# Optimization experiments

Hardware: AMD Instinct MI355X
Metric: run time of the kernel (lower is better)

## Reference

```python
import jax, jax.numpy as jnp
import numpy as np

WS = (7, 7, 7)          # window size (S, H, W)
NUM_HEADS = 6
DIM = 192
B_, NW = 128, 32        # total windows, windows per image (mask dim)
N = WS[0] * WS[1] * WS[2]  # 343 tokens per window


def _relative_position_index():
    # Faithful replica of the torch __init__ logic (incl. indexing='xy' and
    # the 3*W1-1 / 2*W1-1 multipliers).
    cs = np.arange(WS[0]); ch = np.arange(WS[1]); cw = np.arange(WS[2])
    coords = np.stack(np.meshgrid(cs, ch, cw, indexing='xy'))  # (3, Wh, Ws, Ww)
    cf = coords.reshape(3, -1)                                  # (3, N)
    rel = cf[:, :, None] - cf[:, None, :]                       # (3, N, N)
    rel = rel.transpose(1, 2, 0).astype(np.int64)               # (N, N, 3)
    rel[:, :, 0] += WS[0] - 1
    rel[:, :, 1] += WS[1] - 1
    rel[:, :, 2] += WS[2] - 1
    rel[:, :, 0] *= 3 * WS[1] - 1
    rel[:, :, 1] *= 2 * WS[1] - 1
    return rel.sum(-1)                                          # (N, N) int


def setup_inputs() -> dict:
    key = jax.random.key(0)
    ks = jax.random.split(key, 6)
    C = DIM
    x = jax.random.normal(ks[0], (B_, N, C), dtype=jnp.float32)
    mask = jax.random.normal(ks[1], (NW, N, N), dtype=jnp.float32)
    qkv_w = jax.random.normal(ks[2], (3 * C, C), dtype=jnp.float32) * 0.02
    qkv_b = jnp.zeros((3 * C,), dtype=jnp.float32)
    proj_w = jax.random.normal(ks[3], (C, C), dtype=jnp.float32) * 0.02
    proj_b = jnp.zeros((C,), dtype=jnp.float32)
    table_len = (2 * WS[0] - 1) * (2 * WS[1] - 1) * (2 * WS[2] - 1)
    rpb_table = jax.random.normal(ks[4], (table_len, NUM_HEADS), dtype=jnp.float32) * 0.02
    rel_index = jnp.asarray(_relative_position_index(), dtype=jnp.int32)
    return {"x": x, "mask": mask, "qkv_w": qkv_w, "qkv_b": qkv_b,
            "proj_w": proj_w, "proj_b": proj_b, "rpb_table": rpb_table,
            "rel_index": rel_index}


def reference(x, mask, qkv_w, qkv_b, proj_w, proj_b, rpb_table, rel_index):
    B, n, C = x.shape
    H = NUM_HEADS
    hd = C // H
    scale = hd ** (-0.5)
    qkv = x @ qkv_w.T + qkv_b                      # (B, N, 3C)
    qkv = qkv.reshape(B, n, 3, H, hd).transpose(2, 0, 3, 1, 4)  # (3, B, H, N, hd)
    q, k, v = qkv[0] * scale, qkv[1], qkv[2]
    attn = jnp.einsum('bhnd,bhmd->bhnm', q, k)     # (B, H, N, N)
    bias = rpb_table[rel_index.reshape(-1)].reshape(n, n, H)
    attn = attn + bias.transpose(2, 0, 1)[None]    # (B, H, N, N)
    nW = mask.shape[0]
    attn = attn.reshape(B // nW, nW, H, n, n) + mask[None, :, None]
    attn = jax.nn.softmax(attn.reshape(B, H, n, n), axis=-1)
    out = jnp.einsum('bhnm,bhmd->bhnd', attn, v)   # (B, H, N, hd)
    out = out.transpose(0, 2, 1, 3).reshape(B, n, C)
    return out @ proj_w.T + proj_b
```

## Files before the change

### kernel.cpp

```cpp
#include <hip/hip_runtime.h>
#include <hip/hip_fp16.h>
#include <hip/hip_bf16.h>
#include <stdint.h>

#define WN 343
#define NH 6
#define HD 32
#define CD 192
#define NB 128
#define NWM 32
#define BMROW 352
#define BMSLICE (11*16*BMROW)
#define BMKC (16*BMROW)
#define LOG2E 1.4426950408889634f

typedef __attribute__((ext_vector_type(8))) short short8;
typedef __attribute__((ext_vector_type(4))) float f32x4;

__device__ __forceinline__ unsigned short f2bf(float f) {
  union { float f; uint32_t u; } v; v.f = f;
  uint32_t r = v.u + 0x7fffu + ((v.u >> 16) & 1u);
  return (unsigned short)(r >> 16);
}

__device__ __forceinline__ uint32_t pk2bf(float a, float b) {
  __hip_bfloat162 h = __float22bfloat162_rn(make_float2(a, b));
  return *(uint32_t*)&h;
}

__device__ __forceinline__ uint32_t pkh2(float a, float b) {
  __half2 h; h.x = __float2half(a); h.y = __float2half(b);
  return *(uint32_t*)&h;
}

typedef const __attribute__((address_space(1))) unsigned int* gas_ptr;
typedef __attribute__((address_space(3))) unsigned int* las_ptr;
__device__ __forceinline__ void gload16(const unsigned short* g, unsigned short* l) {
  __builtin_amdgcn_global_load_lds((gas_ptr)(const void*)g, (las_ptr)(void*)l, 16, 0, 0);
}

__global__ __launch_bounds__(256) void prep_kernel(
    const float* __restrict__ wq, const float* __restrict__ wp,
    unsigned short* __restrict__ wqb, unsigned short* __restrict__ wpb,
    const int* __restrict__ rel, const float* __restrict__ rpb,
    const float* __restrict__ mask, uint32_t* __restrict__ bP,
    uint32_t* __restrict__ mP, const float* __restrict__ x,
    unsigned short* __restrict__ xb) {
  __shared__ float M[88][33];
  const int bid = blockIdx.x;
  const int tid = threadIdx.x;
  if (bid < 264) {
    const int h = bid / 44;
    const int rem = bid - h * 44;
    const int kc = rem >> 2;
    const int g = rem & 3;
    const int n0 = g * 88;
    const int k0 = kc * 32;
    for (int idx = tid; idx < 88 * 32; idx += 256) {
      int nl = idx >> 5, k = idx & 31;
      int n = n0 + nl;
      int nc = (n < WN) ? n : (WN - 1);
      M[nl][k] = (k0 + k < WN) ? rpb[rel[nc * WN + k0 + k] * NH + h] * LOG2E
                               : -30000.0f;
    }
    __syncthreads();
    uint32_t* outp = bP + (size_t)h * BMSLICE + (size_t)kc * BMKC;
    if (tid < 88) {
      const int nl = tid;
      const int n = n0 + nl;
#pragma unroll
      for (int quad = 0; quad < 4; ++quad) {
        uint4 o;
        o.x = pkh2(M[nl][quad * 8 + 0], M[nl][quad * 8 + 4]);
        o.y = pkh2(M[nl][quad * 8 + 1], M[nl][quad * 8 + 5]);
        o.z = pkh2(M[nl][quad * 8 + 2], M[nl][quad * 8 + 6]);
        o.w = pkh2(M[nl][quad * 8 + 3], M[nl][quad * 8 + 7]);
        *(uint4*)(outp + ((size_t)quad * 352 + n) * 4) = o;
      }
    }
    return;
  }
  int cb = bid - 264;
  if (cb < 352) {
    const int wdx = cb / 11;
    const int kc = cb - wdx * 11;
    const int k0 = kc * 32;
    const float* mw = mask + (size_t)wdx * (WN * WN);
    uint32_t* outp = mP + (size_t)wdx * BMSLICE + (size_t)kc * BMKC;
#pragma unroll
    for (int quad = 0; quad < 4; ++quad) {
      const int q8 = quad * 8;
#pragma unroll
      for (int j = 0; j < 2; ++j) {
        int n = tid + 256 * j;
        if (n < 352) {
          float v[8];
#pragma unroll
          for (int i = 0; i < 8; ++i) {
            int kk = k0 + q8 + i;
            v[i] = (n < WN && kk < WN) ? mw[n * WN + kk] * LOG2E : 0.0f;
          }
          uint4 o;
          o.x = pkh2(v[0], v[4]);
          o.y = pkh2(v[1], v[5]);
          o.z = pkh2(v[2], v[6]);
          o.w = pkh2(v[3], v[7]);
          *(uint4*)(outp + ((size_t)quad * 352 + n) * 4) = o;
        }
      }
    }
    return;
  }
  cb -= 352;
  if (cb < 54) {
    int g = cb * 256 + tid;
    int sk = g / 768; int rem = g - sk * 768;
    int row = rem >> 2; int cc = rem & 3;
    int s = sk / 6; int kt = sk - s * 6;
    int lch = cc ^ ((row >> 1) & 3);
    const float* src = wq + (size_t)(s * 192 + row) * CD + kt * 32 + lch * 8;
    f32x4 a = *(const f32x4*)src;
    f32x4 b = *(const f32x4*)(src + 4);
    union { short8 v8; uint32_t d[4]; } pk;
    pk.d[0] = pk2bf(a[0], a[1]);
    pk.d[1] = pk2bf(a[2], a[3]);
    pk.d[2] = pk2bf(b[0], b[1]);
    pk.d[3] = pk2bf(b[2], b[3]);
    *(short8*)(wqb + (size_t)g * 8) = pk.v8;
    return;
  }
  cb -= 54;
  if (cb < 18) {
    int g = cb * 256 + tid;
    int kt = g / 768; int rem = g - kt * 768;
    int row = rem >> 2; int cc = rem & 3;
    int lch = cc ^ ((row >> 1) & 3);
    const float* src = wp + (size_t)row * CD + kt * 32 + lch * 8;
    f32x4 a = *(const f32x4*)src;
    f32x4 b = *(const f32x4*)(src + 4);
    union { short8 v8; uint32_t d[4]; } pk;
    pk.d[0] = pk2bf(a[0], a[1]);
    pk.d[1] = pk2bf(a[2], a[3]);
    pk.d[2] = pk2bf(b[0], b[1]);
    pk.d[3] = pk2bf(b[2], b[3]);
    *(short8*)(wpb + (size_t)g * 8) = pk.v8;
    return;
  }
  cb -= 18;
  size_t gx = (size_t)cb * 256 + tid;
  int tile = (int)(gx >> 9); int rem = (int)(gx & 511);
  int row = rem >> 2; int cc = rem & 3;
  int mb = tile / 6; int kt = tile - mb * 6;
  int lch = cc ^ ((row >> 1) & 3);
  const float* src = x + ((size_t)mb * 128 + row) * CD + kt * 32 + lch * 8;
  f32x4 a = *(const f32x4*)src;
  f32x4 b = *(const f32x4*)(src + 4);
  union { short8 v8; uint32_t d[4]; } pk;
  pk.d[0] = pk2bf(a[0], a[1]);
  pk.d[1] = pk2bf(a[2], a[3]);
  pk.d[2] = pk2bf(b[0], b[1]);
  pk.d[3] = pk2bf(b[2], b[3]);
  *(short8*)(xb + gx * 8) = pk.v8;
}

__global__ __launch_bounds__(256) void qkv_kernel(
    const unsigned short* __restrict__ xb, const unsigned short* __restrict__ wqb,
    const float* __restrict__ bvec,
    unsigned short* __restrict__ qb, unsigned short* __restrict__ kb,
    unsigned short* __restrict__ vb) {
  __shared__ __align__(16) unsigned short SL[10240];
  unsigned short* XL = SL;
  unsigned short* WL = SL + 4096;
  const int tid = threadIdx.x;
  const int wave = tid >> 6, lane = tid & 63;
  const int quad = lane >> 4, c = lane & 15;
  const int m0 = blockIdx.x * 128;
  const int s = blockIdx.y;
  const int chk = (quad ^ ((c >> 1) & 3)) * 8;

  f32x4 acc[2][12];
#pragma unroll
  for (int i = 0; i < 2; ++i)
#pragma unroll
    for (int j = 0; j < 12; ++j) acc[i][j] = (f32x4){0.f, 0.f, 0.f, 0.f};

  const size_t xt0 = (size_t)blockIdx.x * 6;
  const size_t wt0 = (size_t)s * 6;
  for (int kt = 0; kt < 6; ++kt) {
    const unsigned short* gx = xb + ((xt0 + kt) << 12) + tid * 8;
    const unsigned short* gw = wqb + (wt0 + kt) * 6144 + tid * 8;
    unsigned short* lx = XL + (size_t)wave * 512;
    unsigned short* lw = WL + (size_t)wave * 512;
    gload16(gx, lx);
    gload16(gx + 2048, lx + 2048);
    gload16(gw, lw);
    gload16(gw + 2048, lw + 2048);
    gload16(gw + 4096, lw + 4096);
    __syncthreads();
    short8 af0 = *(const short8*)&XL[(wave * 32 + c) * 32 + chk];
    short8 af1 = *(const short8*)&XL[(wave * 32 + 16 + c) * 32 + chk];
#pragma unroll
    for (int j = 0; j < 12; ++j) {
      short8 bfr = *(const short8*)&WL[(j * 16 + c) * 32 + chk];
      acc[0][j] = __builtin_amdgcn_mfma_f32_16x16x32_bf16(af0, bfr, acc[0][j], 0, 0, 0);
      acc[1][j] = __builtin_amdgcn_mfma_f32_16x16x32_bf16(af1, bfr, acc[1][j], 0, 0, 0);
    }
    __syncthreads();
  }

  const float qscale = 0.25503486f;
  unsigned short* dst = (s == 0) ? qb : ((s == 1) ? kb : vb);
  const float scl = (s == 0) ? qscale : 1.0f;
  const int n0 = s * 192;
  unsigned short* Lh0 = SL;
  unsigned short* Lh1 = SL + 4608;
  for (int hh = 0; hh < 3; ++hh) {
    __syncthreads();
#pragma unroll
    for (int jj = 0; jj < 4; ++jj) {
      int j = hh * 4 + jj;
      int hl = jj >> 1;
      int dd = (jj & 1) * 16 + c;
      float bn = bvec[n0 + j * 16 + c];
      unsigned short* L = hl ? Lh1 : Lh0;
#pragma unroll
      for (int i = 0; i < 2; ++i)
#pragma unroll
        for (int r = 0; r < 4; ++r) {
          int m = wave * 32 + i * 16 + quad * 4 + r;
          L[m * 36 + dd] = f2bf((acc[i][j][r] + bn) * scl);
        }
    }
    __syncthreads();
    const int m = tid & 127;
    const int hl = tid >> 7;
    const int M = m0 + m;
    const int b = M / WN;
    const int tok = M - b * WN;
    const int h = hh * 2 + hl;
    const unsigned short* L = hl ? Lh1 : Lh0;
    unsigned short* drow = dst + (((size_t)b * NH + h) * WN + tok) * HD;
#pragma unroll
    for (int t2 = 0; t2 < 4; ++t2) {
      int d0 = t2 * 8;
      *(short8*)&drow[d0] = *(const short8*)&L[m * 36 + d0];
    }
  }
}

__global__ __launch_bounds__(512) void attn_kernel(
    const unsigned short* __restrict__ qb, const unsigned short* __restrict__ kb,
    const unsigned short* __restrict__ vb, const uint32_t* __restrict__ biasP,
    const uint32_t* __restrict__ maskP, unsigned short* __restrict__ ob) {
  __shared__ __align__(16) unsigned short Ks[352][40];
  __shared__ __align__(16) unsigned short Vt[HD][360];
  const int bid = blockIdx.x;
  const int job = (bid & 7) * 96 + (bid >> 3);
  const int wdx = job / 24;
  const int inner = job - wdx * 24;
  const int h = inner >> 2;
  const int b = (inner & 3) * 32 + wdx;
  const int tid = threadIdx.x;
  const int wave = tid >> 6, lane = tid & 63;
  const int quad = lane >> 4, c = lane & 15;
  const size_t base = ((size_t)b * NH + h) * (WN * HD);
  const unsigned short* q = qb + base;
  const unsigned short* k = kb + base;
  const unsigned short* v = vb + base;
  const uint32_t* bS = biasP + (size_t)h * BMSLICE;
  const uint32_t* mS = maskP + (size_t)wdx * BMSLICE;

  for (int t = tid; t < WN * 4; t += 512) {
    int r = t >> 2, ch = t & 3;
    int kk = r & 31;
    int row = (r & ~31) + 16 * ((kk >> 2) & 1) + 4 * (kk >> 3) + (kk & 3);
    *(short8*)&Ks[row][ch * 8] = *(const short8*)(k + r * HD + ch * 8);
  }
  for (int t = tid; t < 9 * 32; t += 512) {
    int kg = WN + (t >> 5);
    int kk = kg & 31;
    int row = (kg & ~31) + 16 * ((kk >> 2) & 1) + 4 * (kk >> 3) + (kk & 3);
    Ks[row][t & 31] = 0;
  }
  for (int t = tid; t < WN; t += 512) {
#pragma unroll
    for (int ch = 0; ch < 4; ++ch) {
      short8 vv = *(const short8*)(v + t * HD + ch * 8);
#pragma unroll
      for (int j = 0; j < 8; ++j) Vt[ch * 8 + j][t] = vv[j];
    }
  }
  for (int t = tid; t < 9 * 32; t += 512) {
    Vt[t & 31][WN + (t >> 5)] = 0;
  }
  __syncthreads();

  union { short8 v8; uint32_t d[4]; } on;
  on.d[0] = on.d[1] = on.d[2] = on.d[3] = 0x3F803F80u;

  for (int qt = wave; qt < 22; qt += 8) {
    const int q0 = qt * 16;
    int qr = q0 + c; if (qr > WN - 1) qr = WN - 1;
    const short8 qf = *(const short8*)(q + qr * HD + quad * 8);
    const uint32_t* bRow = bS + ((size_t)quad * 352 + q0 + c) * 4;
    const uint32_t* mRow = mS + ((size_t)quad * 352 + q0 + c) * 4;

    f32x4 o0 = (f32x4){0.f, 0.f, 0.f, 0.f};
    f32x4 o1 = (f32x4){0.f, 0.f, 0.f, 0.f};
    f32x4 accl = (f32x4){0.f, 0.f, 0.f, 0.f};
    uint4 bw = *(const uint4*)bRow;
    uint4 mw = *(const uint4*)mRow;
#pragma unroll 1
    for (int kc = 0; kc < 11; ++kc) {
      const int kcn = (kc < 10) ? kc + 1 : 10;
      uint4 bwN = *(const uint4*)(bRow + (size_t)kcn * BMKC);
      uint4 mwN = *(const uint4*)(mRow + (size_t)kcn * BMKC);
      f32x4 cc0, cc1;
      {
        __half2 s2; float2 f;
        s2 = __hadd2(*(__half2*)&bw.x, *(__half2*)&mw.x);
        f = __half22float2(s2); cc0[0] = f.x; cc1[0] = f.y;
        s2 = __hadd2(*(__half2*)&bw.y, *(__half2*)&mw.y);
        f = __half22float2(s2); cc0[1] = f.x; cc1[1] = f.y;
        s2 = __hadd2(*(__half2*)&bw.z, *(__half2*)&mw.z);
        f = __half22float2(s2); cc0[2] = f.x; cc1[2] = f.y;
        s2 = __hadd2(*(__half2*)&bw.w, *(__half2*)&mw.w);
        f = __half22float2(s2); cc0[3] = f.x; cc1[3] = f.y;
      }
      const int k0 = kc * 32;
      short8 kf0 = *(const short8*)&Ks[k0 + c][quad * 8];
      short8 kf1 = *(const short8*)&Ks[k0 + 16 + c][quad * 8];
      __builtin_amdgcn_s_setprio(1);
      f32x4 s0 = __builtin_amdgcn_mfma_f32_16x16x32_bf16(kf0, qf, cc0, 0, 0, 0);
      f32x4 s1 = __builtin_amdgcn_mfma_f32_16x16x32_bf16(kf1, qf, cc1, 0, 0, 0);
      __builtin_amdgcn_s_setprio(0);
      float p0 = __builtin_amdgcn_exp2f(s0[0]), p1 = __builtin_amdgcn_exp2f(s0[1]);
      float p2 = __builtin_amdgcn_exp2f(s0[2]), p3 = __builtin_amdgcn_exp2f(s0[3]);
      float p4 = __builtin_amdgcn_exp2f(s1[0]), p5 = __builtin_amdgcn_exp2f(s1[1]);
      float p6 = __builtin_amdgcn_exp2f(s1[2]), p7 = __builtin_amdgcn_exp2f(s1[3]);
      union { short8 v8; uint32_t d[4]; } pf;
      pf.d[0] = pk2bf(p0, p1);
      pf.d[1] = pk2bf(p2, p3);
      pf.d[2] = pk2bf(p4, p5);
      pf.d[3] = pk2bf(p6, p7);
      short8 vf0 = *(const short8*)&Vt[c][k0 + quad * 8];
      short8 vf1 = *(const short8*)&Vt[16 + c][k0 + quad * 8];
      __builtin_amdgcn_s_setprio(1);
      o0 = __builtin_amdgcn_mfma_f32_16x16x32_bf16(pf.v8, vf0, o0, 0, 0, 0);
      o1 = __builtin_amdgcn_mfma_f32_16x16x32_bf16(pf.v8, vf1, o1, 0, 0, 0);
      accl = __builtin_amdgcn_mfma_f32_16x16x32_bf16(pf.v8, on.v8, accl, 0, 0, 0);
      __builtin_amdgcn_s_setprio(0);
      bw = bwN; mw = mwN;
    }

#pragma unroll
    for (int r = 0; r < 4; ++r) {
      int n = q0 + quad * 4 + r;
      if (n < WN) {
        float inv = 1.0f / accl[r];
        int M = b * WN + n;
        int rloc = M & 127;
        int xr = (rloc >> 1) & 3;
        size_t base2 = (((size_t)(M >> 7) * 6 + h) << 12) + rloc * 32;
        ob[base2 + (((c >> 3) ^ xr) << 3) + (c & 7)] = f2bf(o0[r] * inv);
        ob[base2 + ((((c >> 3) | 2) ^ xr) << 3) + (c & 7)] = f2bf(o1[r] * inv);
      }
    }
  }
}

__global__ __launch_bounds__(256) void proj_kernel(
    const unsigned short* __restrict__ obp, const unsigned short* __restrict__ wpb,
    const float* __restrict__ bvec, float* __restrict__ out) {
  __shared__ __align__(16) unsigned short SL[8192];
  unsigned short* XL = SL;
  unsigned short* WL = SL + 2048;
  const int tid = threadIdx.x;
  const int wave = tid >> 6, lane = tid & 63;
  const int quad = lane >> 4, c = lane & 15;
  const int m0 = blockIdx.x * 64;
  const int mb = blockIdx.x >> 1;
  const int r0 = (blockIdx.x & 1) * 64;
  const int chk = (quad ^ ((c >> 1) & 3)) * 8;

  f32x4 acc[12];
#pragma unroll
  for (int j = 0; j < 12; ++j) acc[j] = (f32x4){0.f, 0.f, 0.f, 0.f};

  for (int kt = 0; kt < 6; ++kt) {
    const unsigned short* gx =
        obp + (((size_t)mb * 6 + kt) << 12) + r0 * 32 + tid * 8;
    const unsigned short* gw = wpb + (size_t)kt * 6144 + tid * 8;
    unsigned short* lx = XL + (size_t)wave * 512;
    unsigned short* lw = WL + (size_t)wave * 512;
    gload16(gx, lx);
    gload16(gw, lw);
    gload16(gw + 2048, lw + 2048);
    gload16(gw + 4096, lw + 4096);
    __syncthreads();
    short8 af = *(const short8*)&XL[(wave * 16 + c) * 32 + chk];
#pragma unroll
    for (int j = 0; j < 12; ++j) {
      short8 bfr = *(const short8*)&WL[(j * 16 + c) * 32 + chk];
      acc[j] = __builtin_amdgcn_mfma_f32_16x16x32_bf16(af, bfr, acc[j], 0, 0, 0);
    }
    __syncthreads();
  }

#pragma unroll
  for (int j = 0; j < 12; ++j) {
    int col = j * 16 + c;
    float bn = bvec[col];
#pragma unroll
    for (int r = 0; r < 4; ++r) {
      int m = m0 + wave * 16 + quad * 4 + r;
      out[(size_t)m * CD + col] = acc[j][r] + bn;
    }
  }
}

extern "C" void kernel_launch(void* const* d_in, const int* in_sizes, int n_in,
                              void* d_out, int out_size, void* d_ws, size_t ws_size,
                              hipStream_t stream) {
  const float* x      = (const float*)d_in[0];
  const float* mask   = (const float*)d_in[1];
  const float* qkv_w  = (const float*)d_in[2];
  const float* qkv_b  = (const float*)d_in[3];
  const float* proj_w = (const float*)d_in[4];
  const float* proj_b = (const float*)d_in[5];
  const float* rpb    = (const float*)d_in[6];
  const int*   rel    = (const int*)d_in[7];
  float* out = (float*)d_out;

  char* ws = (char*)d_ws;
  uint32_t* biasP = (uint32_t*)ws;
  size_t off = 1486848;
  uint32_t* maskP = (uint32_t*)(ws + off); off += 7929856;
  unsigned short* qb = (unsigned short*)(ws + off); off += 16859136;
  unsigned short* kb = (unsigned short*)(ws + off); off += 16859136;
  unsigned short* vb = (unsigned short*)(ws + off); off += 16859136;
  unsigned short* wqb = (unsigned short*)(ws + off); off += 221184;
  unsigned short* wpb = (unsigned short*)(ws + off); off += 73728;
  unsigned short* xb  = (unsigned short*)(ws + off); off += 16859136;
  unsigned short* obuf = xb;

  hipLaunchKernelGGL(prep_kernel, dim3(264 + 352 + 54 + 18 + 4116), dim3(256),
                     0, stream,
                     qkv_w, proj_w, wqb, wpb, rel, rpb, mask, biasP, maskP, x, xb);
  hipLaunchKernelGGL(qkv_kernel, dim3(343, 3), dim3(256), 0, stream,
                     xb, wqb, qkv_b, qb, kb, vb);
  hipLaunchKernelGGL(attn_kernel, dim3(NH * NB), dim3(512), 0, stream,
                     qb, kb, vb, biasP, maskP, obuf);
  hipLaunchKernelGGL(proj_kernel, dim3(686), dim3(256), 0, stream,
                     obuf, wpb, proj_b, out);
}
```

Before: 215.8 us.

## Double-buffer LDS tiles in QKV and projection GEMMs to overlap loads with MFMA

The QKV and output-projection GEMM kernels now use two LDS buffers. The next K-tile is issued with global_load_lds while the current tile feeds the MFMAs, and a custom wait-plus-barrier replaces the two syncthreads per iteration. The attention loop also swaps its clamped next-chunk index for a running pointer increment, so the last iteration prefetches one chunk past the end. In exchange, LDS use per block doubles, which may lower occupancy, and that final prefetch reads past the bias/mask slice.

```diff
diff --git a/kernel.cpp b/kernel.cpp
--- a/kernel.cpp
+++ b/kernel.cpp
@@ -37,6 +37,13 @@
 typedef __attribute__((address_space(3))) unsigned int* las_ptr;
 __device__ __forceinline__ void gload16(const unsigned short* g, unsigned short* l) {
   __builtin_amdgcn_global_load_lds((gas_ptr)(const void*)g, (las_ptr)(void*)l, 16, 0, 0);
+}
+
+__device__ __forceinline__ void pipe_bar() {
+  asm volatile("s_waitcnt vmcnt(0) lgkmcnt(0)" ::: "memory");
+  __builtin_amdgcn_sched_barrier(0);
+  __builtin_amdgcn_s_barrier();
+  __builtin_amdgcn_sched_barrier(0);
 }
 
 __global__ __launch_bounds__(256) void prep_kernel(
@@ -168,9 +175,7 @@
     const float* __restrict__ bvec,
     unsigned short* __restrict__ qb, unsigned short* __restrict__ kb,
     unsigned short* __restrict__ vb) {
-  __shared__ __align__(16) unsigned short SL[10240];
-  unsigned short* XL = SL;
-  unsigned short* WL = SL + 4096;
+  __shared__ __align__(16) unsigned short SL[20480];
   const int tid = threadIdx.x;
   const int wave = tid >> 6, lane = tid & 63;
   const int quad = lane >> 4, c = lane & 15;
@@ -186,26 +191,43 @@
 
   const size_t xt0 = (size_t)blockIdx.x * 6;
   const size_t wt0 = (size_t)s * 6;
-  for (int kt = 0; kt < 6; ++kt) {
+
+  auto STAGE = [&](unsigned short* buf, int kt) {
     const unsigned short* gx = xb + ((xt0 + kt) << 12) + tid * 8;
     const unsigned short* gw = wqb + (wt0 + kt) * 6144 + tid * 8;
-    unsigned short* lx = XL + (size_t)wave * 512;
-    unsigned short* lw = WL + (size_t)wave * 512;
+    unsigned short* lx = buf + (size_t)wave * 512;
+    unsigned short* lw = buf + 4096 + (size_t)wave * 512;
     gload16(gx, lx);
     gload16(gx + 2048, lx + 2048);
     gload16(gw, lw);
     gload16(gw + 2048, lw + 2048);
     gload16(gw + 4096, lw + 4096);
-    __syncthreads();
-    short8 af0 = *(const short8*)&XL[(wave * 32 + c) * 32 + chk];
-    short8 af1 = *(const short8*)&XL[(wave * 32 + 16 + c) * 32 + chk];
+  };
+  auto COMPUTE = [&](const unsigned short* buf) {
+    const unsigned short* XLb = buf;
+    const unsigned short* WLb = buf + 4096;
+    short8 af0 = *(const short8*)&XLb[(wave * 32 + c) * 32 + chk];
+    short8 af1 = *(const short8*)&XLb[(wave * 32 + 16 + c) * 32 + chk];
 #pragma unroll
     for (int j = 0; j < 12; ++j) {
-      short8 bfr = *(const short8*)&WL[(j * 16 + c) * 32 + chk];
+      short8 bfr = *(const short8*)&WLb[(j * 16 + c) * 32 + chk];
       acc[0][j] = __builtin_amdgcn_mfma_f32_16x16x32_bf16(af0, bfr, acc[0][j], 0, 0, 0);
       acc[1][j] = __builtin_amdgcn_mfma_f32_16x16x32_bf16(af1, bfr, acc[1][j], 0, 0, 0);
     }
-    __syncthreads();
+  };
+
+  unsigned short* B0 = SL;
+  unsigned short* B1 = SL + 10240;
+  STAGE(B0, 0);
+  pipe_bar();
+#pragma unroll
+  for (int p = 0; p < 3; ++p) {
+    STAGE(B1, 2 * p + 1);
+    COMPUTE(B0);
+    pipe_bar();
+    if (p < 2) STAGE(B0, 2 * p + 2);
+    COMPUTE(B1);
+    pipe_bar();
   }
 
   const float qscale = 0.25503486f;
@@ -302,19 +324,19 @@
     const int q0 = qt * 16;
     int qr = q0 + c; if (qr > WN - 1) qr = WN - 1;
     const short8 qf = *(const short8*)(q + qr * HD + quad * 8);
-    const uint32_t* bRow = bS + ((size_t)quad * 352 + q0 + c) * 4;
-    const uint32_t* mRow = mS + ((size_t)quad * 352 + q0 + c) * 4;
+    const uint32_t* bPtr = bS + ((size_t)quad * 352 + q0 + c) * 4;
+    const uint32_t* mPtr = mS + ((size_t)quad * 352 + q0 + c) * 4;
 
     f32x4 o0 = (f32x4){0.f, 0.f, 0.f, 0.f};
     f32x4 o1 = (f32x4){0.f, 0.f, 0.f, 0.f};
     f32x4 accl = (f32x4){0.f, 0.f, 0.f, 0.f};
-    uint4 bw = *(const uint4*)bRow;
-    uint4 mw = *(const uint4*)mRow;
+    uint4 bw = *(const uint4*)bPtr;
+    uint4 mw = *(const uint4*)mPtr;
 #pragma unroll 1
     for (int kc = 0; kc < 11; ++kc) {
-      const int kcn = (kc < 10) ? kc + 1 : 10;
-      uint4 bwN = *(const uint4*)(bRow + (size_t)kcn * BMKC);
-      uint4 mwN = *(const uint4*)(mRow + (size_t)kcn * BMKC);
+      bPtr += BMKC; mPtr += BMKC;
+      uint4 bwN = *(const uint4*)bPtr;
+      uint4 mwN = *(const uint4*)mPtr;
       f32x4 cc0, cc1;
       {
         __half2 s2; float2 f;
@@ -372,9 +394,7 @@
 __global__ __launch_bounds__(256) void proj_kernel(
     const unsigned short* __restrict__ obp, const unsigned short* __restrict__ wpb,
     const float* __restrict__ bvec, float* __restrict__ out) {
-  __shared__ __align__(16) unsigned short SL[8192];
-  unsigned short* XL = SL;
-  unsigned short* WL = SL + 2048;
+  __shared__ __align__(16) unsigned short SL[16384];
   const int tid = threadIdx.x;
   const int wave = tid >> 6, lane = tid & 63;
   const int quad = lane >> 4, c = lane & 15;
@@ -387,24 +407,40 @@
 #pragma unroll
   for (int j = 0; j < 12; ++j) acc[j] = (f32x4){0.f, 0.f, 0.f, 0.f};
 
-  for (int kt = 0; kt < 6; ++kt) {
+  auto STAGE = [&](unsigned short* buf, int kt) {
     const unsigned short* gx =
         obp + (((size_t)mb * 6 + kt) << 12) + r0 * 32 + tid * 8;
     const unsigned short* gw = wpb + (size_t)kt * 6144 + tid * 8;
-    unsigned short* lx = XL + (size_t)wave * 512;
-    unsigned short* lw = WL + (size_t)wave * 512;
+    unsigned short* lx = buf + (size_t)wave * 512;
+    unsigned short* lw = buf + 2048 + (size_t)wave * 512;
     gload16(gx, lx);
     gload16(gw, lw);
     gload16(gw + 2048, lw + 2048);
     gload16(gw + 4096, lw + 4096);
-    __syncthreads();
-    short8 af = *(const short8*)&XL[(wave * 16 + c) * 32 + chk];
+  };
+  auto COMPUTE = [&](const unsigned short* buf) {
+    const unsigned short* XLb = buf;
+    const unsigned short* WLb = buf + 2048;
+    short8 af = *(const short8*)&XLb[(wave * 16 + c) * 32 + chk];
 #pragma unroll
     for (int j = 0; j < 12; ++j) {
-      short8 bfr = *(const short8*)&WL[(j * 16 + c) * 32 + chk];
+      short8 bfr = *(const short8*)&WLb[(j * 16 + c) * 32 + chk];
       acc[j] = __builtin_amdgcn_mfma_f32_16x16x32_bf16(af, bfr, acc[j], 0, 0, 0);
     }
-    __syncthreads();
+  };
+
+  unsigned short* B0 = SL;
+  unsigned short* B1 = SL + 8192;
+  STAGE(B0, 0);
+  pipe_bar();
+#pragma unroll
+  for (int p = 0; p < 3; ++p) {
+    STAGE(B1, 2 * p + 1);
+    COMPUTE(B0);
+    pipe_bar();
+    if (p < 2) STAGE(B0, 2 * p + 2);
+    COMPUTE(B1);
+    pipe_bar();
   }
 
 #pragma unroll
```

Result: no change. 211.9 us (-1.8%).
